# Kernel tuning notes

Measured on AMD Instinct MI355X. Metric: run time of the kernel, lower is better.

The kernel has to match this reference:

```python
import jax, jax.numpy as jnp
import numpy as np

NUM_HEADS = 16
ROPE_BASE = 10000.0


def _rotate_half(x):
    x1 = x[..., ::2]
    x2 = x[..., 1::2]
    return jnp.stack((-x2, x1), axis=-1).reshape(x.shape)


def _rope_tables(seq_len, head_dim, dtype):
    inv_freq = 1.0 / (ROPE_BASE ** (jnp.arange(0, head_dim, 2, dtype=jnp.float32) / head_dim))
    t = jnp.arange(seq_len, dtype=jnp.float32)
    freqs = jnp.outer(t, inv_freq)            # [S, head_dim//2]
    emb = jnp.concatenate((freqs, freqs), -1)  # [S, head_dim]
    return jnp.cos(emb).astype(dtype), jnp.sin(emb).astype(dtype)


def setup_inputs() -> dict:
    key = jax.random.key(0)
    ks = jax.random.split(key, 5)
    B, S, H = 1, 4096, 1024
    scale = 1.0 / np.sqrt(H)
    return {
        "x": jax.random.normal(ks[0], (B, S, H), jnp.float32),
        "Wq": jax.random.normal(ks[1], (H, H), jnp.float32) * scale,
        "Wk": jax.random.normal(ks[2], (H, H), jnp.float32) * scale,
        "Wv": jax.random.normal(ks[3], (H, H), jnp.float32) * scale,
        "Wo": jax.random.normal(ks[4], (H, H), jnp.float32) * scale,
        "attention_mask": jnp.ones((B, S), jnp.int32),
    }


def reference(x, Wq, Wk, Wv, Wo, attention_mask):
    B, S, H = x.shape
    hd = H // NUM_HEADS

    def split_heads(t):  # [B,S,H] -> [B,nh,S,hd]
        return t.reshape(B, S, NUM_HEADS, hd).transpose(0, 2, 1, 3)

    q = split_heads(x @ Wq)
    k = split_heads(x @ Wk)
    v = split_heads(x @ Wv)

    cos, sin = _rope_tables(S, hd, x.dtype)
    cos = cos[None, None]  # [1,1,S,hd]
    sin = sin[None, None]
    q = q * cos + _rotate_half(q) * sin
    k = k * cos + _rotate_half(k) * sin

    scores = jnp.einsum("bhqd,bhkd->bhqk", q, k) / jnp.sqrt(jnp.asarray(hd, x.dtype))
    mask = attention_mask.reshape(B, 1, 1, S)
    scores = jnp.where(mask == 0, jnp.finfo(x.dtype).min, scores)
    probs = jax.nn.softmax(scores, axis=-1)
    ctx = jnp.einsum("bhqk,bhkd->bhqd", probs, v)
    ctx = ctx.transpose(0, 2, 1, 3).reshape(B, S, H)
    return ctx @ Wo
```

## Files before the change

### kernel.cpp

```cpp
#include <hip/hip_runtime.h>
#include <cstdint>
#include <cstddef>

#define S_LEN 4096
#define NHEADS 16
#define HD 64
#define HDIM 1024

typedef _Float16 f16x8 __attribute__((ext_vector_type(8)));
typedef _Float16 f16x4 __attribute__((ext_vector_type(4)));
typedef __fp16 h16x2 __attribute__((ext_vector_type(2)));
typedef float f32x4 __attribute__((ext_vector_type(4)));
typedef unsigned char uchar;
typedef unsigned int u32;

__device__ __forceinline__ f32x4 mfma16h(f16x8 a, f16x8 b, f32x4 c) {
    return __builtin_amdgcn_mfma_f32_16x16x32_f16(a, b, c, 0, 0, 0);
}
__device__ __forceinline__ void async16(void* lds, const void* g) {
    __builtin_amdgcn_global_load_lds(
        (const __attribute__((address_space(1))) u32*)g,
        (__attribute__((address_space(3))) u32*)lds, 16, 0, 0);
}


__global__ __launch_bounds__(256) void pack_x(const float* __restrict__ X,
                                              uchar* __restrict__ P,
                                              const int* __restrict__ M,
                                              _Float16* __restrict__ FM16)
{
    int id = blockIdx.x * 256 + threadIdx.x;
    int m = id >> 7, g = id & 127;
    int kc = g >> 3, b = g & 7;
    float v[8];
    *(float4*)&v[0] = *(const float4*)&X[(size_t)m * HDIM + kc * 64 + b * 8];
    *(float4*)&v[4] = *(const float4*)&X[(size_t)m * HDIM + kc * 64 + b * 8 + 4];
    __align__(16) _Float16 h[8];
    #pragma unroll
    for (int i = 0; i < 8; i++) h[i] = (_Float16)v[i];
    size_t base = ((size_t)(m * 16 + kc)) * 128 + (size_t)((b ^ (m & 7)) * 16);
    *(uint4*)(P + base) = *(const uint4*)h;
    if (id < S_LEN) FM16[id] = (_Float16)((M[id] == 0) ? 0.0f : 1.0f);
}

__global__ __launch_bounds__(256) void pack_w4(
    const float* __restrict__ W0, const float* __restrict__ W1,
    const float* __restrict__ W2, const float* __restrict__ W3,
    uchar* __restrict__ P)
{
    int id = blockIdx.x * 256 + threadIdx.x;
    int wsel = id >> 17;
    int lid  = id & 131071;
    int g = lid >> 10, n = lid & 1023;
    int kc = g >> 3, b = g & 7;
    const float* W = (wsel == 0) ? W0 : (wsel == 1) ? W1 : (wsel == 2) ? W2 : W3;
    uchar* dst = P + (size_t)wsel * 2097152;
    float v[8];
    #pragma unroll
    for (int j = 0; j < 8; j++)
        v[j] = W[(size_t)(kc * 64 + b * 8 + j) * HDIM + n];
    __align__(16) _Float16 h[8];
    #pragma unroll
    for (int i = 0; i < 8; i++) h[i] = (_Float16)v[i];
    size_t base = ((size_t)(n * 16 + kc)) * 128 + (size_t)((b ^ (n & 7)) * 16);
    *(uint4*)(dst + base) = *(const uint4*)h;
}

__global__ __launch_bounds__(256) void gemm_f16(
    const uchar* __restrict__ Ap, const uchar* __restrict__ Bp,
    float* __restrict__ C, int head_major)
{
    __shared__ __align__(16) uchar AB[65536];
    const int t = threadIdx.x, lane = t & 63, w = t >> 6;
    const int quad = lane >> 4, l15 = lane & 15, x7 = l15 & 7;
    const int m0 = blockIdx.y * 128, n0 = blockIdx.x * 128;
    const int wm = (w >> 1) * 64, wn = (w & 1) * 64;

    f32x4 acc[4][4];
    const f32x4 zero4 = {0.0f, 0.0f, 0.0f, 0.0f};
    #pragma unroll
    for (int mt = 0; mt < 4; mt++)
        #pragma unroll
        for (int nt = 0; nt < 4; nt++) acc[mt][nt] = zero4;

    #pragma unroll
    for (int i = 0; i < 4; i++) {
        int idx = i * 256 + t;
        int row = idx >> 3, blk = idx & 7;
        int ldso = (idx & ~63) * 16;
        async16(AB + ldso,         Ap + ((size_t)((m0 + row) * 16 + 0)) * 128 + blk * 16);
        async16(AB + 16384 + ldso, Bp + ((size_t)((n0 + row) * 16 + 0)) * 128 + blk * 16);
    }

    for (int kc = 0; kc < 16; kc++) {
        uchar* As = AB + (kc & 1) * 32768;
        uchar* Bs = As + 16384;
        __syncthreads();
        if (kc + 1 < 16) {
            uchar* An = AB + ((kc + 1) & 1) * 32768;
            #pragma unroll
            for (int i = 0; i < 4; i++) {
                int idx = i * 256 + t;
                int row = idx >> 3, blk = idx & 7;
                int ldso = (idx & ~63) * 16;
                async16(An + ldso,
                        Ap + ((size_t)((m0 + row) * 16 + kc + 1)) * 128 + blk * 16);
                async16(An + 16384 + ldso,
                        Bp + ((size_t)((n0 + row) * 16 + kc + 1)) * 128 + blk * 16);
            }
        }
        #pragma unroll
        for (int ks = 0; ks < 2; ks++) {
            const int phys = ((ks * 4 + quad) ^ x7) * 16;
            f16x8 ah[4];
            #pragma unroll
            for (int mt = 0; mt < 4; mt++)
                ah[mt] = *(const f16x8*)(As + (size_t)(wm + mt * 16 + l15) * 128 + phys);
            #pragma unroll
            for (int nt = 0; nt < 4; nt++) {
                f16x8 bh = *(const f16x8*)(Bs + (size_t)(wn + nt * 16 + l15) * 128 + phys);
                #pragma unroll
                for (int mt = 0; mt < 4; mt++)
                    acc[mt][nt] = mfma16h(ah[mt], bh, acc[mt][nt]);
            }
        }
    }

    #pragma unroll
    for (int mt = 0; mt < 4; mt++)
        #pragma unroll
        for (int nt = 0; nt < 4; nt++)
            #pragma unroll
            for (int r = 0; r < 4; r++) {
                int m = m0 + wm + mt * 16 + quad * 4 + r;
                int n = n0 + wn + nt * 16 + l15;
                float val = acc[mt][nt][r];
                if (head_major) {
                    int hh = n >> 6, d = n & 63;
                    C[((size_t)hh * S_LEN + m) * HD + d] = val;
                } else {
                    C[(size_t)m * HDIM + n] = val;
                }
            }
}

__global__ __launch_bounds__(256) void rope_pack(const float* __restrict__ QKVf,
                                                 uchar* __restrict__ Qg,
                                                 uchar* __restrict__ Kg)
{
    int id = blockIdx.x * 256 + threadIdx.x;
    int g  = id & 7;
    int s  = (id >> 3) & (S_LEN - 1);
    int hb = id >> 15;
    const float* src = QKVf + (size_t)hb * (S_LEN * HD) + (size_t)s * HD + g * 8;
    float v[8];
    *(float4*)&v[0] = *(const float4*)&src[0];
    *(float4*)&v[4] = *(const float4*)&src[4];

    const float L32 = 13.287712379549449f / 32.0f;
    float out[8];
    #pragma unroll
    for (int u = 0; u < 4; u++) {
        int de = g * 8 + 2 * u;
        float ae = (float)s * exp2f(-(float)(de & 31) * L32);
        float ao = (float)s * exp2f(-(float)((de + 1) & 31) * L32);
        float ce = __cosf(ae), se = __sinf(ae);
        float co = __cosf(ao), so = __sinf(ao);
        float xe = v[2 * u], xo = v[2 * u + 1];
        out[2 * u]     = xe * ce - xo * se;
        out[2 * u + 1] = xo * co + xe * so;
    }
    const bool isQ = hb < 16;
    const float scale = isQ ? 0.18033688011112042f : 1.0f;
    __align__(16) _Float16 h[8];
    #pragma unroll
    for (int i = 0; i < 8; i++) h[i] = (_Float16)(out[i] * scale);
    uchar* dst = (isQ ? Qg : Kg);
    size_t base = ((size_t)((hb & 15) * S_LEN + s)) * 128 + (size_t)((g ^ (s & 7)) * 16);
    *(uint4*)(dst + base) = *(const uint4*)h;
}

__global__ __launch_bounds__(256) void v_pack(const float* __restrict__ Vf,
                                              const int* __restrict__ M,
                                              uchar* __restrict__ Vg)
{
    int id = blockIdx.x * 256 + threadIdx.x;
    int d    = id & 63;
    int kg   = (id >> 6) & 15;
    int kc2  = (id >> 10) & 31;
    int head = id >> 15;
    __align__(16) _Float16 hv[8];
    #pragma unroll
    for (int j = 0; j < 8; j++) {
        int key = kc2 * 128 + kg * 8 + j;
        float x = Vf[(size_t)head * (S_LEN * HD) + (size_t)key * HD + d];
        hv[j] = (M[key] == 0) ? (_Float16)0.0f : (_Float16)x;
    }
    size_t base = ((size_t)(head * 32 + kc2)) * 16384 + (size_t)d * 256 +
                  (size_t)((kg ^ (d & 7)) * 16);
    *(uint4*)(Vg + base) = *(const uint4*)hv;
}

#define ISSUE_K(CC, KB)                                                        \
  {                                                                            \
    const uchar* ks_ = kgb + (size_t)(CC) * 16384;                             \
    async16((KB),        ks_ + l16);                                           \
    async16((KB) + 1024, ks_ + 1024 + l16);                                    \
    async16((KB) + 2048, ks_ + 2048 + l16);                                    \
    async16((KB) + 3072, ks_ + 3072 + l16);                                    \
  }
#define ISSUE_V(CC)                                                            \
  {                                                                            \
    const uchar* vs_ = vgb + (size_t)(CC) * 16384;                             \
    async16(VB,        vs_ + voff);                                            \
    async16(VB + 1024, vs_ + 4096 + voff);                                     \
    async16(VB + 2048, vs_ + 8192 + voff);                                     \
    async16(VB + 3072, vs_ + 12288 + voff);                                    \
  }

#define ATTN_STEP(CC, KB, TOPC, MIDC, FLG)                                     \
  {                                                                            \
    asm volatile("s_waitcnt vmcnt(" TOPC ")" ::: "memory");                    \
    f32x4 s0[4], s1[4];                                                        \
    _Pragma("unroll")                                                          \
    for (int qt = 0; qt < 4; qt++) { s0[qt] = zero4; s1[qt] = zero4; }         \
    _Pragma("unroll")                                                          \
    for (int ks = 0; ks < 2; ks++) {                                           \
      const int phys_ = ((ks * 4 + quad) ^ x7) * 16;                           \
      f16x8 kf0 = *(const f16x8*)((KB) + (size_t)l15 * 128 + phys_);           \
      f16x8 kf1 = *(const f16x8*)((KB) + (size_t)(16 + l15) * 128 + phys_);    \
      _Pragma("unroll")                                                        \
      for (int qt = 0; qt < 4; qt++) {                                         \
        s0[qt] = mfma16h(kf0, qf[qt][ks], s0[qt]);                             \
        s1[qt] = mfma16h(kf1, qf[qt][ks], s1[qt]);                             \
      }                                                                        \
    }                                                                          \
    uchar* Pw_ = (KB);                                                         \
    _Pragma("unroll")                                                          \
    for (int qt = 0; qt < 4; qt++) {                                           \
      h16x2 c01 = __builtin_amdgcn_cvt_pkrtz(exp2f(s0[qt][0]), exp2f(s0[qt][1])); \
      h16x2 c23 = __builtin_amdgcn_cvt_pkrtz(exp2f(s0[qt][2]), exp2f(s0[qt][3])); \
      h16x2 c45 = __builtin_amdgcn_cvt_pkrtz(exp2f(s1[qt][0]), exp2f(s1[qt][1])); \
      h16x2 c67 = __builtin_amdgcn_cvt_pkrtz(exp2f(s1[qt][2]), exp2f(s1[qt][3])); \
      uint2 a0 = make_uint2(__builtin_bit_cast(u32, c01),                      \
                            __builtin_bit_cast(u32, c23));                     \
      uint2 a1 = make_uint2(__builtin_bit_cast(u32, c45),                      \
                            __builtin_bit_cast(u32, c67));                     \
      uchar* prow_ = Pw_ + (size_t)(qt * 16 + l15) * 64 + (quad & 1) * 8;      \
      *(uint2*)(prow_ + ((((quad >> 1)) ^ psw) * 16))     = a0;                \
      *(uint2*)(prow_ + (((2 + (quad >> 1)) ^ psw) * 16)) = a1;                \
    }                                                                          \
    asm volatile("s_waitcnt vmcnt(" MIDC ")" ::: "memory");                    \
    {                                                                          \
      f16x8 pb[4];                                                             \
      _Pragma("unroll")                                                        \
      for (int qt = 0; qt < 4; qt++)                                           \
        pb[qt] = *(const f16x8*)(Pw_ + (size_t)(qt * 16 + l15) * 64 +          \
                                 ((quad ^ psw) * 16));                         \
      _Pragma("unroll")                                                        \
      for (int dt = 0; dt < 4; dt++) {                                         \
        f16x8 va = *(const f16x8*)(VB + (size_t)(dt * 16 + l15) * 64 + vrd);   \
        _Pragma("unroll")                                                      \
        for (int qt = 0; qt < 4; qt++)                                         \
          o[dt][qt] = mfma16h(va, pb[qt], o[dt][qt]);                          \
      }                                                                        \
      _Pragma("unroll")                                                        \
      for (int qt = 0; qt < 4; qt++)                                           \
        lacc[qt] = mfma16h((FLG), pb[qt], lacc[qt]);                           \
    }                                                                          \
    asm volatile("s_waitcnt lgkmcnt(0)" ::: "memory");                         \
    if ((CC) + 1 < 32) ISSUE_V((CC) + 1);                                      \
    if ((CC) + 2 < 32) {                                                       \
      ISSUE_K((CC) + 2, KB);                                                   \
      (FLG) = *(const f16x8*)(fmw + (size_t)((CC) + 2) * 256);                 \
    }                                                                          \
  }

__global__ __launch_bounds__(256, 2) void attn8b(
    const uchar* __restrict__ Qg, const uchar* __restrict__ Kg,
    const uchar* __restrict__ Vg, const uchar* __restrict__ fm16,
    uchar* __restrict__ CTXp)
{
    __shared__ __align__(16) uchar arena[49152];
    __shared__ float Lsh[4][64];
    __shared__ float Lfin[64];
    float* Os = (float*)arena;

    const int t    = threadIdx.x;
    const int lane = t & 63;
    const int w    = t >> 6;
    const int quad = lane >> 4;
    const int l15  = lane & 15;
    const int x7   = l15 & 7;
    const int hh   = blockIdx.y;
    const int m0   = blockIdx.x * 64;

    const uchar* qgb = Qg + (size_t)hh * (S_LEN * 128);
    const uchar* kgb = Kg + (size_t)hh * (S_LEN * 128) + (size_t)w * 4096;
    const uchar* vgb = Vg + (size_t)hh * 32 * 16384;
    const uchar* fmw = fm16 + w * 64 + quad * 16;

    uchar* WB = arena + w * 12288;
    uchar* K0 = WB;
    uchar* K1 = WB + 4096;
    uchar* VB = WB + 8192;

    const int l16 = lane * 16;
    const int vphys = ((w * 4 + ((lane & 3) ^ ((lane >> 2) & 3))) ^ ((lane >> 2) & 7));
    const int voff  = (lane >> 2) * 256 + vphys * 16;
    const int vrd   = (quad ^ (l15 & 3)) * 16;
    const int psw   = (l15 >> 1) & 3;

    f16x8 qf[4][2];
    #pragma unroll
    for (int qt = 0; qt < 4; qt++)
        #pragma unroll
        for (int ks = 0; ks < 2; ks++)
            qf[qt][ks] = *(const f16x8*)(qgb + (size_t)(m0 + qt * 16 + l15) * 128 +
                                         (size_t)(((ks * 4 + quad) ^ x7) * 16));

    f32x4 o[4][4], lacc[4];
    const f32x4 zero4 = {0.0f, 0.0f, 0.0f, 0.0f};
    #pragma unroll
    for (int dt = 0; dt < 4; dt++)
        #pragma unroll
        for (int qt = 0; qt < 4; qt++) o[dt][qt] = zero4;
    #pragma unroll
    for (int qt = 0; qt < 4; qt++) lacc[qt] = zero4;

    ISSUE_K(0, K0);
    ISSUE_V(0);
    f16x8 flagA = *(const f16x8*)(fmw);
    f16x8 flagB = *(const f16x8*)(fmw + 256);
    ISSUE_K(1, K1);

    for (int c = 0; c < 30; c += 2) {
        ATTN_STEP(c,     K0, "8", "4", flagA);
        ATTN_STEP(c + 1, K1, "8", "4", flagB);
    }
    ATTN_STEP(30, K0, "8", "4", flagA);
    ATTN_STEP(31, K1, "4", "0", flagB);

    __syncthreads();
    if (quad == 0) {
        #pragma unroll
        for (int qt = 0; qt < 4; qt++)
            Lsh[w][qt * 16 + l15] = lacc[qt][0];
    }
    __syncthreads();
    if (t < 64)
        Lfin[t] = Lsh[0][t] + Lsh[1][t] + Lsh[2][t] + Lsh[3][t];
    __syncthreads();

    for (int wv = 0; wv < 4; wv++) {
        if (w == wv) {
            #pragma unroll
            for (int dt = 0; dt < 4; dt++)
                #pragma unroll
                for (int qt = 0; qt < 4; qt++)
                    #pragma unroll
                    for (int r = 0; r < 4; r++) {
                        int q = qt * 16 + l15;
                        int d = dt * 16 + quad * 4 + r;
                        float val = o[dt][qt][r];
                        if (wv == 0) Os[q * 68 + d] = val;
                        else         Os[q * 68 + d] += val;
                    }
        }
        __syncthreads();
    }

    #pragma unroll
    for (int i = 0; i < 4; i++) {
        int idx = t + 256 * i;
        int q   = idx >> 4;
        int c4  = (idx & 15) * 4;
        float inv = 1.0f / Lfin[q];
        float4 v = *(const float4*)&Os[q * 68 + c4];
        int m = m0 + q;
        __align__(8) _Float16 h[4];
        h[0] = (_Float16)(v.x * inv);
        h[1] = (_Float16)(v.y * inv);
        h[2] = (_Float16)(v.z * inv);
        h[3] = (_Float16)(v.w * inv);
        size_t base = ((size_t)(m * 16 + hh)) * 128 +
                      (size_t)((((c4 >> 3) ^ (m & 7))) * 16) + (c4 & 7) * 2;
        *(ushort4*)(CTXp + base) = *(const ushort4*)h;
    }
}

extern "C" void kernel_launch(void* const* d_in, const int* in_sizes, int n_in,
                              void* d_out, int out_size, void* d_ws, size_t ws_size,
                              hipStream_t stream)
{
    const float* x   = (const float*)d_in[0];
    const float* Wq  = (const float*)d_in[1];
    const float* Wk  = (const float*)d_in[2];
    const float* Wv  = (const float*)d_in[3];
    const float* Wo  = (const float*)d_in[4];
    const int* amask = (const int*)d_in[5];
    float* out = (float*)d_out;
    float* ws  = (float*)d_ws;

    float* QKVf = ws;
    uchar* Xp   = (uchar*)ws + 50331648;
    uchar* Wt4  = (uchar*)ws + 58720256;
    uchar* Vg   = (uchar*)ws + 67108864;
    _Float16* Fm16 = (_Float16*)((uchar*)ws + 75497472);
    uchar* Qg   = Xp;
    uchar* Kg   = (uchar*)ws + 33554432;
    uchar* CTXp = (uchar*)ws;

    dim3 blk(256);

    pack_x<<<2048, blk, 0, stream>>>(x, Xp, amask, Fm16);
    pack_w4<<<2048, blk, 0, stream>>>(Wq, Wk, Wv, Wo, Wt4);

    gemm_f16<<<dim3(24, 32), blk, 0, stream>>>(Xp, Wt4, QKVf, 1);

    v_pack<<<2048, blk, 0, stream>>>(QKVf + 8388608, amask, Vg);
    rope_pack<<<4096, blk, 0, stream>>>(QKVf, Qg, Kg);

    attn8b<<<dim3(S_LEN / 64, NHEADS), blk, 0, stream>>>(Qg, Kg, Vg,
                                                         (const uchar*)Fm16, CTXp);

    gemm_f16<<<dim3(8, 32), blk, 0, stream>>>(CTXp, Wt4 + 6291456, out, 0);
}
```

Measured before the change: 264.3 us.

## Keep softmax probabilities in registers by permuting V and mask key order

Drops the LDS round-trip for the P matrix in the attention loop: the exp'd scores are packed straight into MFMA B-operand registers. To make the register layout match, the V pack kernel and the mask-vector pack now permute key order so the PV MFMA sees keys in the matching lane order. This removes LDS writes and reads plus their bank traffic per step, at the cost of more scattered 8-byte stores in v_pack and a correctness dependence on the permutation being exact.

```diff
diff --git a/kernel.cpp b/kernel.cpp
--- a/kernel.cpp
+++ b/kernel.cpp
@@ -40,7 +40,13 @@
     for (int i = 0; i < 8; i++) h[i] = (_Float16)v[i];
     size_t base = ((size_t)(m * 16 + kc)) * 128 + (size_t)((b ^ (m & 7)) * 16);
     *(uint4*)(P + base) = *(const uint4*)h;
-    if (id < S_LEN) FM16[id] = (_Float16)((M[id] == 0) ? 0.0f : 1.0f);
+    if (id < S_LEN) {
+        int c = id >> 7, k128 = id & 127;
+        int w = k128 >> 5, k32 = k128 & 31;
+        int q = (k32 >> 2) & 3, kt = k32 >> 4, r = k32 & 3;
+        FM16[c * 128 + w * 32 + q * 8 + kt * 4 + r] =
+            (_Float16)((M[id] == 0) ? 0.0f : 1.0f);
+    }
 }
 
 __global__ __launch_bounds__(256) void pack_w4(
@@ -196,9 +202,18 @@
         float x = Vf[(size_t)head * (S_LEN * HD) + (size_t)key * HD + d];
         hv[j] = (M[key] == 0) ? (_Float16)0.0f : (_Float16)x;
     }
-    size_t base = ((size_t)(head * 32 + kc2)) * 16384 + (size_t)d * 256 +
-                  (size_t)((kg ^ (d & 7)) * 16);
-    *(uint4*)(Vg + base) = *(const uint4*)hv;
+    int wv  = kg >> 2;
+    int kgm = kg & 3;
+    int kt  = kgm >> 1;
+    int qA  = (kgm * 2) & 3;
+    int qB  = (kgm * 2 + 1) & 3;
+    int slotA = wv * 32 + qA * 8 + kt * 4;
+    int slotB = wv * 32 + qB * 8 + kt * 4;
+    size_t row = ((size_t)(head * 32 + kc2)) * 16384 + (size_t)d * 256;
+    *(ushort4*)(Vg + row + (size_t)(((slotA >> 3) ^ (d & 7)) * 16 + (slotA & 7) * 2))
+        = *(const ushort4*)&hv[0];
+    *(ushort4*)(Vg + row + (size_t)(((slotB >> 3) ^ (d & 7)) * 16 + (slotB & 7) * 2))
+        = *(const ushort4*)&hv[4];
 }
 
 #define ISSUE_K(CC, KB)                                                        \
@@ -235,28 +250,22 @@
         s1[qt] = mfma16h(kf1, qf[qt][ks], s1[qt]);                             \
       }                                                                        \
     }                                                                          \
-    uchar* Pw_ = (KB);                                                         \
+    f16x8 pb[4];                                                               \
     _Pragma("unroll")                                                          \
     for (int qt = 0; qt < 4; qt++) {                                           \
       h16x2 c01 = __builtin_amdgcn_cvt_pkrtz(exp2f(s0[qt][0]), exp2f(s0[qt][1])); \
       h16x2 c23 = __builtin_amdgcn_cvt_pkrtz(exp2f(s0[qt][2]), exp2f(s0[qt][3])); \
       h16x2 c45 = __builtin_amdgcn_cvt_pkrtz(exp2f(s1[qt][0]), exp2f(s1[qt][1])); \
       h16x2 c67 = __builtin_amdgcn_cvt_pkrtz(exp2f(s1[qt][2]), exp2f(s1[qt][3])); \
-      uint2 a0 = make_uint2(__builtin_bit_cast(u32, c01),                      \
-                            __builtin_bit_cast(u32, c23));                     \
-      uint2 a1 = make_uint2(__builtin_bit_cast(u32, c45),                      \
-                            __builtin_bit_cast(u32, c67));                     \
-      uchar* prow_ = Pw_ + (size_t)(qt * 16 + l15) * 64 + (quad & 1) * 8;      \
-      *(uint2*)(prow_ + ((((quad >> 1)) ^ psw) * 16))     = a0;                \
-      *(uint2*)(prow_ + (((2 + (quad >> 1)) ^ psw) * 16)) = a1;                \
+      uint4 pw;                                                                \
+      pw.x = __builtin_bit_cast(u32, c01);                                     \
+      pw.y = __builtin_bit_cast(u32, c23);                                     \
+      pw.z = __builtin_bit_cast(u32, c45);                                     \
+      pw.w = __builtin_bit_cast(u32, c67);                                     \
+      pb[qt] = __builtin_bit_cast(f16x8, pw);                                  \
     }                                                                          \
     asm volatile("s_waitcnt vmcnt(" MIDC ")" ::: "memory");                    \
     {                                                                          \
-      f16x8 pb[4];                                                             \
-      _Pragma("unroll")                                                        \
-      for (int qt = 0; qt < 4; qt++)                                           \
-        pb[qt] = *(const f16x8*)(Pw_ + (size_t)(qt * 16 + l15) * 64 +          \
-                                 ((quad ^ psw) * 16));                         \
       _Pragma("unroll")                                                        \
       for (int dt = 0; dt < 4; dt++) {                                         \
         f16x8 va = *(const f16x8*)(VB + (size_t)(dt * 16 + l15) * 64 + vrd);   \
@@ -276,7 +285,7 @@
     }                                                                          \
   }
 
-__global__ __launch_bounds__(256, 2) void attn8b(
+__global__ __launch_bounds__(256, 2) void attn9(
     const uchar* __restrict__ Qg, const uchar* __restrict__ Kg,
     const uchar* __restrict__ Vg, const uchar* __restrict__ fm16,
     uchar* __restrict__ CTXp)
@@ -309,7 +318,6 @@
     const int vphys = ((w * 4 + ((lane & 3) ^ ((lane >> 2) & 3))) ^ ((lane >> 2) & 7));
     const int voff  = (lane >> 2) * 256 + vphys * 16;
     const int vrd   = (quad ^ (l15 & 3)) * 16;
-    const int psw   = (l15 >> 1) & 3;
 
     f16x8 qf[4][2];
     #pragma unroll
@@ -421,8 +429,8 @@
     v_pack<<<2048, blk, 0, stream>>>(QKVf + 8388608, amask, Vg);
     rope_pack<<<4096, blk, 0, stream>>>(QKVf, Qg, Kg);
 
-    attn8b<<<dim3(S_LEN / 64, NHEADS), blk, 0, stream>>>(Qg, Kg, Vg,
-                                                         (const uchar*)Fm16, CTXp);
+    attn9<<<dim3(S_LEN / 64, NHEADS), blk, 0, stream>>>(Qg, Kg, Vg,
+                                                        (const uchar*)Fm16, CTXp);
 
     gemm_f16<<<dim3(8, 32), blk, 0, stream>>>(CTXp, Wt4 + 6291456, out, 0);
 }
```

Result: faster. 252.4 us (-4.5%).
